# Performance work log

Hardware: AMD Instinct MI355X
Metric: run time of the kernel (lower is better)

Reference implementation:

```python
import jax, jax.numpy as jnp
import numpy as np

N, E, H = 5000, 40000, 8
DIMS = [(258, 512), (516, 256), (262, 128), (136, 20)]  # (in_feature, out_feature) per GATDeformer


def setup_inputs() -> dict:
    key = jax.random.key(0)
    ks = jax.random.split(key, 10)
    s = 0.05
    data = jax.random.normal(ks[0], (N, 10), jnp.float32)
    src = jax.random.randint(ks[1], (E,), 0, N)
    off = jax.random.randint(ks[2], (E,), 1, N)
    edge_idx = jnp.stack([src, (src + off) % N]).astype(jnp.int32)  # no self loops by construction
    inp = {
        'data': data,
        'edge_idx': edge_idx,
        'W0': jax.random.normal(ks[3], (10, 256), jnp.float32) * s,
        'b0': jnp.zeros((256,), jnp.float32),
    }
    for i, (din, dout) in enumerate(DIMS, start=1):
        k = jax.random.split(ks[3 + i], 3)
        inp[f'W{i}'] = jax.random.normal(k[0], (din, H * dout), jnp.float32) * s
        inp[f'asrc{i}'] = jax.random.normal(k[1], (H, dout), jnp.float32) * s
        inp[f'adst{i}'] = jax.random.normal(k[2], (H, dout), jnp.float32) * s
        inp[f'bias{i}'] = jnp.zeros((dout,), jnp.float32)
    return inp


def _gat(x, src, dst, W, a_s, a_d, b):
    """PyG GATConv (concat=False): returns (mean-over-heads output + bias, alpha [E',H])."""
    Hh, C = a_s.shape
    h = (x @ W).reshape(N, Hh, C)                               # [N,H,C]
    e_s = jnp.einsum('nhc,hc->nh', h, a_s)                      # [N,H]
    e_d = jnp.einsum('nhc,hc->nh', h, a_d)
    logits = jax.nn.leaky_relu(e_s[src] + e_d[dst], 0.2)        # [E',H]
    m = jax.ops.segment_max(logits, dst, num_segments=N)        # segment softmax over incoming edges
    ex = jnp.exp(logits - m[dst])
    alpha = ex / jax.ops.segment_sum(ex, dst, num_segments=N)[dst]
    out = jax.ops.segment_sum(alpha[:, :, None] * h[src], dst, num_segments=N)  # [N,H,C]
    return out.mean(axis=1) + b, alpha


def _deformer(af, src, dst, W, a_s, a_d, b):
    # find_boundary on the layer input features
    up, down = af[:, 0] == 1.0, af[:, 0] == 0.0
    left, right = af[:, 1] == 0.0, af[:, 1] == 1.0
    feat, alpha = _gat(af, src, dst, W, a_s, a_d, b)
    coord = af[:, :2]
    # second propagate: alpha*0.2 reused to aggregate source coordinates, then mean over heads
    msg = (alpha * 0.2)[:, :, None] * coord[src][:, None, :]    # [E',H,2]
    oc = jax.ops.segment_sum(msg, dst, num_segments=N).mean(axis=1)
    # fix_boundary (sequential overwrite order: up then down, left then right)
    c0 = jnp.where(down, 0.0, jnp.where(up, 1.0, oc[:, 0]))
    c1 = jnp.where(right, 1.0, jnp.where(left, 0.0, oc[:, 1]))
    return jnp.stack([c0, c1], axis=1), jax.nn.selu(feat)


def reference(data, edge_idx, W0, b0, W1, asrc1, adst1, bias1, W2, asrc2, adst2, bias2, W3, asrc3, adst3, bias3, W4, asrc4, adst4, bias4):
    sl = jnp.arange(N, dtype=edge_idx.dtype)
    src = jnp.concatenate([edge_idx[0], sl])   # GATConv add_self_loops=True
    dst = jnp.concatenate([edge_idx[1], sl])
    coord = data[:, :2]
    feat = jax.nn.selu(data @ W0 + b0)
    c1_, f1 = _deformer(jnp.concatenate([coord, feat], 1), src, dst, W1, asrc1, adst1, bias1)
    c2_, f2 = _deformer(jnp.concatenate([c1_, coord, f1], 1), src, dst, W2, asrc2, adst2, bias2)
    c3_, f3 = _deformer(jnp.concatenate([c2_, c1_, coord, f2], 1), src, dst, W3, asrc3, adst3, bias3)
    c4_, _ = _deformer(jnp.concatenate([c3_, c2_, c1_, coord, f3], 1), src, dst, W4, asrc4, adst4, bias4)
    return c4_
```

## Files before the change

### kernel.cpp

```cpp
#include <hip/hip_runtime.h>

#define N_NODES 5000
#define NH 8
#define MAXDEG 128

typedef unsigned short u16;
typedef short bf16x8 __attribute__((ext_vector_type(8)));
typedef float f32x4 __attribute__((ext_vector_type(4)));

static __device__ __forceinline__ float selu_f(float x) {
    const float sc = 1.0507009873554805f;
    const float al = 1.6732632423543772f;
    return x > 0.f ? sc * x : sc * al * (__expf(x) - 1.f);
}

static __device__ __forceinline__ u16 f2bf(float x) {
    union { float f; unsigned u; } v; v.f = x;
    unsigned r = v.u + 0x7fff + ((v.u >> 16) & 1);
    return (u16)(r >> 16);
}

static __device__ __forceinline__ float bf2f(unsigned hi16) {
    union { unsigned u; float f; } v; v.u = hi16 << 16;
    return v.f;
}

#define GL2LDS16(gp, lp)                                                        \
    __builtin_amdgcn_global_load_lds(                                           \
        (const __attribute__((address_space(1))) void*)(gp),                    \
        (__attribute__((address_space(3))) void*)(lp), 16, 0, 0)

#define WAVE_LDS_FENCE() asm volatile("s_waitcnt lgkmcnt(0)" ::: "memory")

__global__ __launch_bounds__(256) void k_prep(
        const float* W1, const float* W2, const float* W3, const float* W4,
        const float* s1, const float* s2, const float* s3, const float* s4,
        const float* d1, const float* d2, const float* d3, const float* d4,
        float* __restrict__ fsAll, float* __restrict__ fdAll,
        u16* T1, u16* T2, u16* T3, int* __restrict__ cnt) {
    const int Ks[4] = {258, 516, 262, 136};
    const int Cs[4] = {512, 256, 128, 20};
    const int NB0 = 16 * 18;
    const int NB1 = 8  * 34;
    const int NB2 = 4  * 18;
    const int NWTR = NB0 + NB1 + NB2;
    int bid = blockIdx.x;
    if (bid < 516) {
        int li = bid / 129;
        int k = (bid % 129) * 4 + (threadIdx.x >> 6);
        int lane = threadIdx.x & 63;
        if (k >= Ks[li]) return;
        const float* W  = (li == 0) ? W1 : (li == 1) ? W2 : (li == 2) ? W3 : W4;
        const float* as = (li == 0) ? s1 : (li == 1) ? s2 : (li == 2) ? s3 : s4;
        const float* ad = (li == 0) ? d1 : (li == 1) ? d2 : (li == 2) ? d3 : d4;
        int C = Cs[li];
        float s[8] = {0.f,0.f,0.f,0.f,0.f,0.f,0.f,0.f};
        float d[8] = {0.f,0.f,0.f,0.f,0.f,0.f,0.f,0.f};
        const float* wr = W + (size_t)k * 8 * C;
        for (int c = lane * 4; c < C; c += 256) {
            #pragma unroll
            for (int h = 0; h < 8; ++h) {
                float4 wv = *(const float4*)(wr + h * C + c);
                float4 sv = *(const float4*)(as + h * C + c);
                float4 dv = *(const float4*)(ad + h * C + c);
                s[h] += wv.x * sv.x + wv.y * sv.y + wv.z * sv.z + wv.w * sv.w;
                d[h] += wv.x * dv.x + wv.y * dv.y + wv.z * dv.z + wv.w * dv.w;
            }
        }
        #pragma unroll
        for (int off = 32; off >= 1; off >>= 1) {
            #pragma unroll
            for (int h = 0; h < 8; ++h) {
                s[h] += __shfl_xor(s[h], off);
                d[h] += __shfl_xor(d[h], off);
            }
        }
        if (lane == 0) {
            float* fo = fsAll + (size_t)li * 516 * 8 + k * 8;
            float* go = fdAll + (size_t)li * 516 * 8 + k * 8;
            #pragma unroll
            for (int h = 0; h < 8; ++h) { fo[h] = s[h]; go[h] = d[h]; }
        }
    } else if (bid < 516 + NWTR) {
        int w = bid - 516;
        int li, rem, nc;
        if (w < NB0)            { li = 0; rem = w;             nc = 16; }
        else if (w < NB0 + NB1) { li = 1; rem = w - NB0;       nc = 8;  }
        else                    { li = 2; rem = w - NB0 - NB1; nc = 4;  }
        const int Kps[3] = {288, 544, 288};
        int C = Cs[li], K = Ks[li], Kp = Kps[li], KK = 8 * Kp;
        int c0 = (rem % nc) * 32;
        int jb = (rem / nc) * 128;
        const float* W = (li == 0) ? W1 : (li == 1) ? W2 : W3;
        u16* Wt2 = (li == 0) ? T1 : (li == 1) ? T2 : T3;
        __shared__ float tile[32][33];
        int t = threadIdx.x;
        int kr = t >> 3, f = t & 7;
        #pragma unroll
        for (int jt = 0; jt < 4; ++jt) {
            int j0 = jb + jt * 32;
            int h = j0 / Kp, k0 = j0 % Kp;
            int gk = k0 + kr;
            float4 v = {0.f, 0.f, 0.f, 0.f};
            if (gk < K) v = *(const float4*)(W + (size_t)gk * (8 * C) + h * C + c0 + f * 4);
            tile[kr][f * 4 + 0] = v.x;
            tile[kr][f * 4 + 1] = v.y;
            tile[kr][f * 4 + 2] = v.z;
            tile[kr][f * 4 + 3] = v.w;
            __syncthreads();
            int cr = kr, kc0 = f * 4;
            ushort4 o;
            o.x = f2bf(tile[kc0 + 0][cr]);
            o.y = f2bf(tile[kc0 + 1][cr]);
            o.z = f2bf(tile[kc0 + 2][cr]);
            o.w = f2bf(tile[kc0 + 3][cr]);
            *(ushort4*)(Wt2 + (size_t)(c0 + cr) * KK + j0 + kc0) = o;
            __syncthreads();
        }
    } else {
        for (int i = threadIdx.x; i < N_NODES; i += 256) cnt[i] = 0;
    }
}

__global__ __launch_bounds__(256) void k_fmf1b(
        const int* __restrict__ ei, int* __restrict__ cnt,
        int* __restrict__ ssrcb, int E, int Esz, int gE,
        const float* __restrict__ data, const float* __restrict__ W0,
        const float* __restrict__ b0,
        const float* __restrict__ fs, const float* __restrict__ fd,
        u16* __restrict__ afb, float* __restrict__ es, float* __restrict__ ed,
        float* __restrict__ c0out) {
    int bid = blockIdx.x, t = threadIdx.x;
    if (bid < gE) {
        int e = bid * 256 + t;
        if (e >= Esz) return;
        int src, dst;
        if (e < E) { src = ei[e]; dst = ei[E + e]; }
        else       { src = e - E; dst = src; }
        int pos = atomicAdd(&cnt[dst], 1);
        if (pos < MAXDEG) ssrcb[dst * MAXDEG + pos] = src;
        return;
    }
    const int FC = 256, K = 258, Kp = 288;
    int n = bid - gE;
    __shared__ float drow[10];
    if (t < 10) drow[t] = data[n * 10 + t];
    __syncthreads();
    float pes[8] = {0.f,0.f,0.f,0.f,0.f,0.f,0.f,0.f};
    float ped[8] = {0.f,0.f,0.f,0.f,0.f,0.f,0.f,0.f};
    u16* rowb = afb + (size_t)n * Kp;
    for (int cf2 = t; 2 * cf2 < FC; cf2 += 256) {
        int cf = 2 * cf2;
        float2 bb = *(const float2*)(b0 + cf);
        float v0 = bb.x, v1 = bb.y;
        #pragma unroll
        for (int k = 0; k < 10; ++k) {
            float2 ww = *(const float2*)(W0 + k * 256 + cf);
            v0 += drow[k] * ww.x;
            v1 += drow[k] * ww.y;
        }
        v0 = selu_f(v0); v1 = selu_f(v1);
        int c = 2 + cf;
        *(unsigned*)(rowb + c) = (unsigned)f2bf(v0) | ((unsigned)f2bf(v1) << 16);
        const float* fsr = fs + c * 8;
        const float* fdr = fd + c * 8;
        #pragma unroll
        for (int h = 0; h < 8; ++h) {
            pes[h] += v0 * fsr[h] + v1 * fsr[8 + h];
            ped[h] += v0 * fdr[h] + v1 * fdr[8 + h];
        }
    }
    if (t < 2) {
        float v = drow[t];
        c0out[n * 2 + t] = v;
        rowb[t] = f2bf(v);
        #pragma unroll
        for (int h = 0; h < 8; ++h) { pes[h] += v * fs[t * 8 + h]; ped[h] += v * fd[t * 8 + h]; }
    }
    for (int c = K + t; c < Kp; c += 256) rowb[c] = 0;
    #pragma unroll
    for (int off = 32; off >= 1; off >>= 1) {
        #pragma unroll
        for (int h = 0; h < 8; ++h) {
            pes[h] += __shfl_xor(pes[h], off);
            ped[h] += __shfl_xor(ped[h], off);
        }
    }
    __shared__ float red[4][16];
    int wv = t >> 6, ln = t & 63;
    if (ln == 0) {
        #pragma unroll
        for (int h = 0; h < 8; ++h) { red[wv][h] = pes[h]; red[wv][8 + h] = ped[h]; }
    }
    __syncthreads();
    if (t < 16) {
        float s = red[0][t] + red[1][t] + red[2][t] + red[3][t];
        if (t < 8) es[n * 8 + t] = s;
        else       ed[n * 8 + (t - 8)] = s;
    }
}

__global__ __launch_bounds__(256) void k_mf(const float* p0, const float* p1,
                                            const float* p2, const float* p3, int np,
                                            const u16* __restrict__ facc,
                                            const float* __restrict__ biasp,
                                            int split, int MN, int FC, int K, int Kp,
                                            const float* __restrict__ fs,
                                            const float* __restrict__ fd,
                                            u16* __restrict__ afb,
                                            float* __restrict__ es, float* __restrict__ ed) {
    int n = blockIdx.x, t = threadIdx.x;
    float pes[8] = {0.f,0.f,0.f,0.f,0.f,0.f,0.f,0.f};
    float ped[8] = {0.f,0.f,0.f,0.f,0.f,0.f,0.f,0.f};
    u16* rowb = afb + (size_t)n * Kp;
    for (int cf2 = t; 2 * cf2 < FC; cf2 += 256) {
        int cf = 2 * cf2;
        float s0 = 0.f, s1 = 0.f;
        for (int z = 0; z < split; ++z) {
            unsigned pr = *(const unsigned*)(facc + (size_t)z * MN + (size_t)n * FC + cf);
            s0 += bf2f(pr & 0xffff);
            s1 += bf2f(pr >> 16);
        }
        float2 bb = *(const float2*)(biasp + cf);
        float v0 = selu_f(s0 * 0.125f + bb.x);
        float v1 = selu_f(s1 * 0.125f + bb.y);
        int c = 2 * np + cf;
        *(unsigned*)(rowb + c) = (unsigned)f2bf(v0) | ((unsigned)f2bf(v1) << 16);
        const float* fsr = fs + c * 8;
        const float* fdr = fd + c * 8;
        #pragma unroll
        for (int h = 0; h < 8; ++h) {
            pes[h] += v0 * fsr[h] + v1 * fsr[8 + h];
            ped[h] += v0 * fdr[h] + v1 * fdr[8 + h];
        }
    }
    if (t < 2 * np) {
        const float* p = (t < 2) ? p0 : (t < 4) ? p1 : (t < 6) ? p2 : p3;
        float v = p[n * 2 + (t & 1)];
        rowb[t] = f2bf(v);
        #pragma unroll
        for (int h = 0; h < 8; ++h) { pes[h] += v * fs[t * 8 + h]; ped[h] += v * fd[t * 8 + h]; }
    }
    for (int c = K + t; c < Kp; c += 256) rowb[c] = 0;
    #pragma unroll
    for (int off = 32; off >= 1; off >>= 1) {
        #pragma unroll
        for (int h = 0; h < 8; ++h) {
            pes[h] += __shfl_xor(pes[h], off);
            ped[h] += __shfl_xor(ped[h], off);
        }
    }
    __shared__ float red[4][16];
    int wv = t >> 6, ln = t & 63;
    if (ln == 0) {
        #pragma unroll
        for (int h = 0; h < 8; ++h) { red[wv][h] = pes[h]; red[wv][8 + h] = ped[h]; }
    }
    __syncthreads();
    if (t < 16) {
        float s = red[0][t] + red[1][t] + red[2][t] + red[3][t];
        if (t < 8) es[n * 8 + t] = s;
        else       ed[n * 8 + (t - 8)] = s;
    }
}

template <int S>
__global__ __launch_bounds__(256) void k_gag2(const float* __restrict__ es,
                            const float* __restrict__ ed,
                            const int* __restrict__ cnt, const int* __restrict__ ssrcb,
                            const float* __restrict__ cprev, const u16* __restrict__ afb,
                            u16* __restrict__ g, float* __restrict__ cnext, int Kp) {
    __shared__ float la_s[4][128 * 8];
    __shared__ int   ls_s[4][128];
    __shared__ float linv_s[4][8];
    int w4 = threadIdx.x >> 6, lane = threadIdx.x & 63;
    int n = blockIdx.x * 4 + w4;
    if (n >= N_NODES) return;
    float* la = la_s[w4];
    int*   ls = ls_s[w4];
    float* linv = linv_s[w4];

    int deg = cnt[n];
    if (deg > MAXDEG) deg = MAXDEG;
    const int* row = ssrcb + (size_t)n * MAXDEG;
    for (int i = lane; i < deg; i += 64) ls[i] = row[i];
    WAVE_LDS_FENCE();

    int h = lane & 7, ei = lane >> 3;
    float edh = ed[n * 8 + h];
    float m = -1e30f;
    for (int b = 0; b < deg; b += 8) {
        int e = b + ei;
        if (e < deg) {
            float x = es[ls[e] * 8 + h] + edh;
            x = x > 0.f ? x : 0.2f * x;
            la[e * 8 + h] = x;
            m = fmaxf(m, x);
        }
    }
    m = fmaxf(m, __shfl_xor(m, 8));
    m = fmaxf(m, __shfl_xor(m, 16));
    m = fmaxf(m, __shfl_xor(m, 32));
    WAVE_LDS_FENCE();
    float ssum = 0.f;
    for (int b = 0; b < deg; b += 8) {
        int e = b + ei;
        if (e < deg) {
            float v = __expf(la[e * 8 + h] - m);
            la[e * 8 + h] = v;
            ssum += v;
        }
    }
    ssum += __shfl_xor(ssum, 8);
    ssum += __shfl_xor(ssum, 16);
    ssum += __shfl_xor(ssum, 32);
    if (lane < 8) linv[lane] = 1.f / ssum;
    WAVE_LDS_FENCE();

    int nW = Kp >> 1;
    float linv8[8];
    #pragma unroll
    for (int h2 = 0; h2 < 8; ++h2) linv8[h2] = linv[h2];

    float acc[8][2 * S];
    #pragma unroll
    for (int h2 = 0; h2 < 8; ++h2)
        #pragma unroll
        for (int s = 0; s < 2 * S; ++s) acc[h2][s] = 0.f;
    int e = 0;
    for (; e + 3 < deg; e += 4) {
        const unsigned* r0 = (const unsigned*)(afb + (size_t)ls[e] * Kp);
        const unsigned* r1 = (const unsigned*)(afb + (size_t)ls[e + 1] * Kp);
        const unsigned* r2 = (const unsigned*)(afb + (size_t)ls[e + 2] * Kp);
        const unsigned* r3 = (const unsigned*)(afb + (size_t)ls[e + 3] * Kp);
        unsigned v0[S], v1[S], v2[S], v3[S];
        #pragma unroll
        for (int s = 0; s < S; ++s) {
            int w = lane + 64 * s;
            bool ok = (w < nW);
            v0[s] = ok ? r0[w] : 0u;
            v1[s] = ok ? r1[w] : 0u;
            v2[s] = ok ? r2[w] : 0u;
            v3[s] = ok ? r3[w] : 0u;
        }
        float a0[8], a1[8], a2[8], a3[8];
        #pragma unroll
        for (int h2 = 0; h2 < 8; ++h2) {
            a0[h2] = la[(e + 0) * 8 + h2];
            a1[h2] = la[(e + 1) * 8 + h2];
            a2[h2] = la[(e + 2) * 8 + h2];
            a3[h2] = la[(e + 3) * 8 + h2];
        }
        #pragma unroll
        for (int s = 0; s < S; ++s) {
            float x0 = bf2f(v0[s] & 0xffff), y0 = bf2f(v0[s] >> 16);
            float x1 = bf2f(v1[s] & 0xffff), y1 = bf2f(v1[s] >> 16);
            float x2 = bf2f(v2[s] & 0xffff), y2 = bf2f(v2[s] >> 16);
            float x3 = bf2f(v3[s] & 0xffff), y3 = bf2f(v3[s] >> 16);
            #pragma unroll
            for (int h2 = 0; h2 < 8; ++h2) {
                acc[h2][2 * s]     += a0[h2] * x0 + a1[h2] * x1 + a2[h2] * x2 + a3[h2] * x3;
                acc[h2][2 * s + 1] += a0[h2] * y0 + a1[h2] * y1 + a2[h2] * y2 + a3[h2] * y3;
            }
        }
    }
    for (; e < deg; ++e) {
        const unsigned* r0 = (const unsigned*)(afb + (size_t)ls[e] * Kp);
        unsigned v0[S];
        #pragma unroll
        for (int s = 0; s < S; ++s) {
            int w = lane + 64 * s;
            v0[s] = (w < nW) ? r0[w] : 0u;
        }
        float a0[8];
        #pragma unroll
        for (int h2 = 0; h2 < 8; ++h2) a0[h2] = la[e * 8 + h2];
        #pragma unroll
        for (int s = 0; s < S; ++s) {
            float x0 = bf2f(v0[s] & 0xffff), y0 = bf2f(v0[s] >> 16);
            #pragma unroll
            for (int h2 = 0; h2 < 8; ++h2) {
                acc[h2][2 * s]     += a0[h2] * x0;
                acc[h2][2 * s + 1] += a0[h2] * y0;
            }
        }
    }
    unsigned* grw = (unsigned*)(g + (size_t)n * 8 * Kp);
    #pragma unroll
    for (int s = 0; s < S; ++s) {
        int w = lane + 64 * s;
        if (w < nW) {
            #pragma unroll
            for (int h2 = 0; h2 < 8; ++h2) {
                float iv = linv8[h2];
                unsigned lo = f2bf(acc[h2][2 * s] * iv);
                unsigned hi = f2bf(acc[h2][2 * s + 1] * iv);
                grw[h2 * nW + w] = lo | (hi << 16);
            }
        }
    }
    float oc0 = 0.f, oc1 = 0.f;
    for (int i = lane; i < deg; i += 64) {
        float wsum = 0.f;
        #pragma unroll
        for (int h2 = 0; h2 < 8; ++h2) wsum += la[i * 8 + h2] * linv8[h2];
        int src = ls[i];
        oc0 += wsum * cprev[src * 2];
        oc1 += wsum * cprev[src * 2 + 1];
    }
    #pragma unroll
    for (int off = 1; off <= 32; off <<= 1) {
        oc0 += __shfl_xor(oc0, off);
        oc1 += __shfl_xor(oc1, off);
    }
    if (lane == 0) {
        oc0 *= 0.025f; oc1 *= 0.025f;
        float a0 = cprev[n * 2], a1 = cprev[n * 2 + 1];
        cnext[n * 2]     = (a0 == 0.f) ? 0.f : ((a0 == 1.f) ? 1.f : oc0);
        cnext[n * 2 + 1] = (a1 == 1.f) ? 1.f : ((a1 == 0.f) ? 0.f : oc1);
    }
}

__global__ __launch_bounds__(256) void k_gemm_s(const u16* __restrict__ A,
                                                const u16* __restrict__ Bt,
                                                u16* __restrict__ facc16,
                                                int M, int KK, int NC, int kchunk, int MN) {
    __shared__ u16 As[3][128 * 32];
    __shared__ u16 Bs[3][128 * 32];
    int tid = threadIdx.x;
    int wave = tid >> 6, lane = tid & 63;
    int bm = blockIdx.y * 128, bn = blockIdx.x * 128, z = blockIdx.z;
    int kbeg = z * kchunk, kend = min(KK, kbeg + kchunk);
    int wm = (wave >> 1) * 64, wn = (wave & 1) * 64;
    int l16 = lane & 15, q = lane >> 4;
    f32x4 acc[4][4] = {};

    int seg0 = wave * 128 + lane;
    int seg1 = seg0 + 64;
    int row0 = seg0 >> 2, sq0 = (seg0 & 3) ^ (row0 & 3);
    int row1 = seg1 >> 2, sq1 = (seg1 & 3) ^ (row1 & 3);
    const u16* ga0 = A  + (size_t)(bm + row0) * KK + sq0 * 8;
    const u16* ga1 = A  + (size_t)(bm + row1) * KK + sq1 * 8;
    const u16* gb0 = Bt + (size_t)(bn + row0) * KK + sq0 * 8;
    const u16* gb1 = Bt + (size_t)(bn + row1) * KK + sq1 * 8;
    int lo0 = (wave * 2 + 0) * 512;
    int lo1 = (wave * 2 + 1) * 512;

#define STAGE_T(buf, kk)                          \
    do {                                          \
        GL2LDS16(ga0 + (kk), &As[buf][lo0]);      \
        GL2LDS16(ga1 + (kk), &As[buf][lo1]);      \
        GL2LDS16(gb0 + (kk), &Bs[buf][lo0]);      \
        GL2LDS16(gb1 + (kk), &Bs[buf][lo1]);      \
    } while (0)

    STAGE_T(0, kbeg);
    if (kbeg + 32 < kend) STAGE_T(1, kbeg + 32);
    int cur = 0;
    for (int k0 = kbeg; k0 < kend; k0 += 32) {
        if (k0 + 64 < kend) {
            int nb = cur + 2; if (nb >= 3) nb -= 3;
            STAGE_T(nb, k0 + 64);
            asm volatile("s_waitcnt vmcnt(8)" ::: "memory");
        } else if (k0 + 32 < kend) {
            asm volatile("s_waitcnt vmcnt(4)" ::: "memory");
        } else {
            asm volatile("s_waitcnt vmcnt(0)" ::: "memory");
        }
        __builtin_amdgcn_s_barrier();
        const u16* Asr = As[cur];
        const u16* Bsr = Bs[cur];
        bf16x8 fa[4], fb[4];
        #pragma unroll
        for (int mi = 0; mi < 4; ++mi) {
            int row = wm + mi * 16 + l16;
            fa[mi] = *(const bf16x8*)(Asr + row * 32 + ((q ^ (row & 3)) * 8));
            int col = wn + mi * 16 + l16;
            fb[mi] = *(const bf16x8*)(Bsr + col * 32 + ((q ^ (col & 3)) * 8));
        }
        #pragma unroll
        for (int mi = 0; mi < 4; ++mi)
            #pragma unroll
            for (int ni = 0; ni < 4; ++ni)
                acc[mi][ni] = __builtin_amdgcn_mfma_f32_16x16x32_bf16(fa[mi], fb[ni], acc[mi][ni], 0, 0, 0);
        __builtin_amdgcn_s_barrier();
        cur += 1; if (cur >= 3) cur -= 3;
    }
#undef STAGE_T
    u16* out = facc16 + (size_t)z * MN;
    #pragma unroll
    for (int mi = 0; mi < 4; ++mi) {
        int row0s = bm + wm + mi * 16 + q * 4;
        #pragma unroll
        for (int ni = 0; ni < 4; ++ni) {
            int col = bn + wn + ni * 16 + l16;
            #pragma unroll
            for (int r = 0; r < 4; ++r) {
                int row = row0s + r;
                if (row < M) out[(size_t)row * NC + col] = f2bf(acc[mi][ni][r]);
            }
        }
    }
}

__global__ void k_final(const float* __restrict__ es, const float* __restrict__ ed,
                        const int* __restrict__ cnt, const int* __restrict__ ssrcb,
                        const float* __restrict__ cprev, float* __restrict__ outp) {
    int wid = (blockIdx.x * blockDim.x + threadIdx.x) >> 6;
    int lane = threadIdx.x & 63;
    if (wid >= N_NODES) return;
    int n = wid;
    int deg = cnt[n];
    if (deg > MAXDEG) deg = MAXDEG;
    const int* row = ssrcb + (size_t)n * MAXDEG;
    int h = lane & 7, ei = lane >> 3;
    float edh = ed[n * 8 + h];
    float m = -1e30f;
    for (int b = 0; b < deg; b += 8) {
        int e = b + ei;
        if (e < deg) {
            int src = row[e];
            float x = es[src * 8 + h] + edh;
            x = x > 0.f ? x : 0.2f * x;
            m = fmaxf(m, x);
        }
    }
    m = fmaxf(m, __shfl_xor(m, 8));
    m = fmaxf(m, __shfl_xor(m, 16));
    m = fmaxf(m, __shfl_xor(m, 32));
    float ssum = 0.f;
    for (int b = 0; b < deg; b += 8) {
        int e = b + ei;
        if (e < deg) {
            int src = row[e];
            float x = es[src * 8 + h] + edh;
            x = x > 0.f ? x : 0.2f * x;
            ssum += __expf(x - m);
        }
    }
    ssum += __shfl_xor(ssum, 8);
    ssum += __shfl_xor(ssum, 16);
    ssum += __shfl_xor(ssum, 32);
    float inv = 1.f / ssum;
    float oc0 = 0.f, oc1 = 0.f;
    for (int b = 0; b < deg; b += 8) {
        int e = b + ei;
        if (e < deg) {
            int src = row[e];
            float x = es[src * 8 + h] + edh;
            x = x > 0.f ? x : 0.2f * x;
            float w = __expf(x - m) * inv;
            w += __shfl_xor(w, 1);
            w += __shfl_xor(w, 2);
            w += __shfl_xor(w, 4);
            if (h == 0) {
                oc0 += w * cprev[src * 2];
                oc1 += w * cprev[src * 2 + 1];
            }
        }
    }
    oc0 += __shfl_xor(oc0, 8);  oc1 += __shfl_xor(oc1, 8);
    oc0 += __shfl_xor(oc0, 16); oc1 += __shfl_xor(oc1, 16);
    oc0 += __shfl_xor(oc0, 32); oc1 += __shfl_xor(oc1, 32);
    if (lane == 0) {
        oc0 *= 0.025f; oc1 *= 0.025f;
        float a0 = cprev[n * 2], a1 = cprev[n * 2 + 1];
        outp[n * 2]     = (a0 == 0.f) ? 0.f : ((a0 == 1.f) ? 1.f : oc0);
        outp[n * 2 + 1] = (a1 == 1.f) ? 1.f : ((a1 == 0.f) ? 0.f : oc1);
    }
}

extern "C" void kernel_launch(void* const* d_in, const int* in_sizes, int n_in,
                              void* d_out, int out_size, void* d_ws, size_t ws_size,
                              hipStream_t stream) {
    const float* data = (const float*)d_in[0];
    const int* ei = (const int*)d_in[1];
    const float* W0 = (const float*)d_in[2];
    const float* b0 = (const float*)d_in[3];
    int E = in_sizes[1] / 2;
    int Esz = E + N_NODES;
    int gE = (Esz + 255) / 256;

    char* wp = (char*)d_ws;
    size_t off = 0;
    auto alloc = [&](size_t bytes) {
        void* p = wp + off;
        off += (bytes + 1023) & ~(size_t)1023;
        return p;
    };
    u16*   g     = (u16*)alloc((size_t)N_NODES * 8 * 576 * 2);
    u16*   T1    = (u16*)alloc((size_t)512 * 8 * 288 * 2);
    u16*   T2    = (u16*)alloc((size_t)256 * 8 * 544 * 2);
    u16*   T3    = (u16*)alloc((size_t)128 * 8 * 288 * 2);
    u16*   facc  = (u16*)alloc((size_t)8 * N_NODES * 512 * 2);
    u16*   afb   = (u16*)alloc((size_t)N_NODES * 576 * 2);
    float* es    = (float*)alloc((size_t)N_NODES * 8 * 4);
    float* ebd   = (float*)alloc((size_t)N_NODES * 8 * 4);
    float* fsAll = (float*)alloc((size_t)4 * 516 * 8 * 4);
    float* fdAll = (float*)alloc((size_t)4 * 516 * 8 * 4);
    float* c0    = (float*)alloc(N_NODES * 2 * 4);
    float* c1    = (float*)alloc(N_NODES * 2 * 4);
    float* c2    = (float*)alloc(N_NODES * 2 * 4);
    float* c3    = (float*)alloc(N_NODES * 2 * 4);
    int* cnt   = (int*)alloc(N_NODES * 4);
    int* ssrcb = (int*)alloc((size_t)N_NODES * MAXDEG * 4);

    struct LP { const float *W, *as, *ad, *bs; int K, C, split; };
    LP L[4] = {
        {(const float*)d_in[4],  (const float*)d_in[5],  (const float*)d_in[6],  (const float*)d_in[7],  258, 512, 4},
        {(const float*)d_in[8],  (const float*)d_in[9],  (const float*)d_in[10], (const float*)d_in[11], 516, 256, 8},
        {(const float*)d_in[12], (const float*)d_in[13], (const float*)d_in[14], (const float*)d_in[15], 262, 128, 8},
        {(const float*)d_in[16], (const float*)d_in[17], (const float*)d_in[18], (const float*)d_in[19], 136, 20, 1},
    };

    k_prep<<<516 + 632 + 1, 256, 0, stream>>>(
        L[0].W, L[1].W, L[2].W, L[3].W,
        L[0].as, L[1].as, L[2].as, L[3].as,
        L[0].ad, L[1].ad, L[2].ad, L[3].ad,
        fsAll, fdAll, T1, T2, T3, cnt);

    k_fmf1b<<<gE + N_NODES, 256, 0, stream>>>(
        ei, cnt, ssrcb, E, Esz, gE,
        data, W0, b0,
        fsAll + 0, fdAll + 0, afb, es, ebd, c0);

    float* cbuf[4] = {c0, c1, c2, c3};
    u16* Tb[3] = {T1, T2, T3};
    int FC[4] = {256, 512, 256, 128};

    for (int li = 0; li < 4; ++li) {
        LP& lp = L[li];
        int Kp = ((lp.K + 31) / 32) * 32;
        int KK = 8 * Kp;

        if (li >= 1) {
            const float* p[4] = {nullptr, nullptr, nullptr, nullptr};
            for (int j = 0; j <= li; ++j) p[j] = cbuf[li - j];
            const float* biasp = L[li - 1].bs;
            int splitp = L[li - 1].split;
            int MNp = N_NODES * FC[li];
            const float* fs = fsAll + (size_t)li * 516 * 8;
            const float* fd = fdAll + (size_t)li * 516 * 8;
            k_mf<<<N_NODES, 256, 0, stream>>>(p[0], p[1], p[2], p[3], li + 1,
                                              facc, biasp, splitp, MNp, FC[li],
                                              lp.K, Kp, fs, fd, afb, es, ebd);
        }
        if (li < 3) {
            int gG = (N_NODES + 3) / 4;
            if (Kp == 544)
                k_gag2<5><<<gG, 256, 0, stream>>>(es, ebd, cnt, ssrcb, cbuf[li], afb,
                                                  g, cbuf[li + 1], Kp);
            else
                k_gag2<3><<<gG, 256, 0, stream>>>(es, ebd, cnt, ssrcb, cbuf[li], afb,
                                                  g, cbuf[li + 1], Kp);
            int MN = N_NODES * lp.C;
            k_gemm_s<<<dim3(lp.C / 128, (N_NODES + 127) / 128, lp.split), 256, 0, stream>>>(
                g, Tb[li], facc, N_NODES, KK, lp.C, KK / lp.split, MN);
        } else {
            k_final<<<(N_NODES + 3) / 4, 256, 0, stream>>>(es, ebd, cnt, ssrcb, cbuf[3],
                                                           (float*)d_out);
        }
    }
}
```

Baseline: 330.6 us.

## Fuse bias/SELU/attention-logit epilogue into GEMM and drop split-K buffer

Removes the separate k_mf kernel and the split-K bf16 partial buffer. The GEMM now runs without K splitting, with a tile-order remap. Its epilogue applies bias and SELU, writes the next layer's bf16 features, and accumulates per-head source/destination logits via shuffles and atomicAdd. The aggregation kernel now computes the coordinate part of the next layer's logits and input row, with ping-pong buffers for features and logits. This saves a launch and a large round-trip through global memory. In exchange, grids without split-K have fewer blocks (as few as 40 for the last layer), the epilogue uses atomics, and the atomic targets rely on being initialized by the aggregation kernel, which adds an ordering dependency.

```diff
diff --git a/kernel.cpp b/kernel.cpp
--- a/kernel.cpp
+++ b/kernel.cpp
@@ -200,76 +200,17 @@
     }
 }
 
-__global__ __launch_bounds__(256) void k_mf(const float* p0, const float* p1,
-                                            const float* p2, const float* p3, int np,
-                                            const u16* __restrict__ facc,
-                                            const float* __restrict__ biasp,
-                                            int split, int MN, int FC, int K, int Kp,
-                                            const float* __restrict__ fs,
-                                            const float* __restrict__ fd,
-                                            u16* __restrict__ afb,
-                                            float* __restrict__ es, float* __restrict__ ed) {
-    int n = blockIdx.x, t = threadIdx.x;
-    float pes[8] = {0.f,0.f,0.f,0.f,0.f,0.f,0.f,0.f};
-    float ped[8] = {0.f,0.f,0.f,0.f,0.f,0.f,0.f,0.f};
-    u16* rowb = afb + (size_t)n * Kp;
-    for (int cf2 = t; 2 * cf2 < FC; cf2 += 256) {
-        int cf = 2 * cf2;
-        float s0 = 0.f, s1 = 0.f;
-        for (int z = 0; z < split; ++z) {
-            unsigned pr = *(const unsigned*)(facc + (size_t)z * MN + (size_t)n * FC + cf);
-            s0 += bf2f(pr & 0xffff);
-            s1 += bf2f(pr >> 16);
-        }
-        float2 bb = *(const float2*)(biasp + cf);
-        float v0 = selu_f(s0 * 0.125f + bb.x);
-        float v1 = selu_f(s1 * 0.125f + bb.y);
-        int c = 2 * np + cf;
-        *(unsigned*)(rowb + c) = (unsigned)f2bf(v0) | ((unsigned)f2bf(v1) << 16);
-        const float* fsr = fs + c * 8;
-        const float* fdr = fd + c * 8;
-        #pragma unroll
-        for (int h = 0; h < 8; ++h) {
-            pes[h] += v0 * fsr[h] + v1 * fsr[8 + h];
-            ped[h] += v0 * fdr[h] + v1 * fdr[8 + h];
-        }
-    }
-    if (t < 2 * np) {
-        const float* p = (t < 2) ? p0 : (t < 4) ? p1 : (t < 6) ? p2 : p3;
-        float v = p[n * 2 + (t & 1)];
-        rowb[t] = f2bf(v);
-        #pragma unroll
-        for (int h = 0; h < 8; ++h) { pes[h] += v * fs[t * 8 + h]; ped[h] += v * fd[t * 8 + h]; }
-    }
-    for (int c = K + t; c < Kp; c += 256) rowb[c] = 0;
-    #pragma unroll
-    for (int off = 32; off >= 1; off >>= 1) {
-        #pragma unroll
-        for (int h = 0; h < 8; ++h) {
-            pes[h] += __shfl_xor(pes[h], off);
-            ped[h] += __shfl_xor(ped[h], off);
-        }
-    }
-    __shared__ float red[4][16];
-    int wv = t >> 6, ln = t & 63;
-    if (ln == 0) {
-        #pragma unroll
-        for (int h = 0; h < 8; ++h) { red[wv][h] = pes[h]; red[wv][8 + h] = ped[h]; }
-    }
-    __syncthreads();
-    if (t < 16) {
-        float s = red[0][t] + red[1][t] + red[2][t] + red[3][t];
-        if (t < 8) es[n * 8 + t] = s;
-        else       ed[n * 8 + (t - 8)] = s;
-    }
-}
-
 template <int S>
-__global__ __launch_bounds__(256) void k_gag2(const float* __restrict__ es,
+__global__ __launch_bounds__(256) void k_gag3(const float* __restrict__ es,
                             const float* __restrict__ ed,
                             const int* __restrict__ cnt, const int* __restrict__ ssrcb,
                             const float* __restrict__ cprev, const u16* __restrict__ afb,
-                            u16* __restrict__ g, float* __restrict__ cnext, int Kp) {
+                            u16* __restrict__ g, float* __restrict__ cnext, int Kp,
+                            int np1, int K1, int Kp1,
+                            const float* __restrict__ fs1, const float* __restrict__ fd1,
+                            float* __restrict__ esN, float* __restrict__ edN,
+                            u16* __restrict__ afbN,
+                            const float* __restrict__ p2, const float* __restrict__ p3) {
     __shared__ float la_s[4][128 * 8];
     __shared__ int   ls_s[4][128];
     __shared__ float linv_s[4][8];
@@ -413,24 +354,54 @@
         oc0 += __shfl_xor(oc0, off);
         oc1 += __shfl_xor(oc1, off);
     }
-    if (lane == 0) {
-        oc0 *= 0.025f; oc1 *= 0.025f;
-        float a0 = cprev[n * 2], a1 = cprev[n * 2 + 1];
-        cnext[n * 2]     = (a0 == 0.f) ? 0.f : ((a0 == 1.f) ? 1.f : oc0);
-        cnext[n * 2 + 1] = (a1 == 1.f) ? 1.f : ((a1 == 0.f) ? 0.f : oc1);
-    }
-}
-
-__global__ __launch_bounds__(256) void k_gemm_s(const u16* __restrict__ A,
+    float a0 = cprev[n * 2], a1 = cprev[n * 2 + 1];
+    float cn0 = (a0 == 0.f) ? 0.f : ((a0 == 1.f) ? 1.f : oc0 * 0.025f);
+    float cn1 = (a1 == 1.f) ? 1.f : ((a1 == 0.f) ? 0.f : oc1 * 0.025f);
+    if (lane == 0) { cnext[n * 2] = cn0; cnext[n * 2 + 1] = cn1; }
+    float cv[8];
+    cv[0] = cn0; cv[1] = cn1;
+    cv[2] = a0;  cv[3] = a1;
+    cv[4] = 0.f; cv[5] = 0.f; cv[6] = 0.f; cv[7] = 0.f;
+    if (np1 >= 3) { cv[4] = p2[n * 2]; cv[5] = p2[n * 2 + 1]; }
+    if (np1 >= 4) { cv[6] = p3[n * 2]; cv[7] = p3[n * 2 + 1]; }
+    if (lane < 8) {
+        float se = 0.f, sd = 0.f;
+        for (int t2 = 0; t2 < 2 * np1; ++t2) {
+            se += cv[t2] * fs1[t2 * 8 + lane];
+            sd += cv[t2] * fd1[t2 * 8 + lane];
+        }
+        esN[n * 8 + lane] = se;
+        edN[n * 8 + lane] = sd;
+    }
+    if (afbN) {
+        if (lane < 2 * np1) afbN[(size_t)n * Kp1 + lane] = f2bf(cv[lane]);
+        for (int c = K1 + lane; c < Kp1; c += 64) afbN[(size_t)n * Kp1 + c] = 0;
+    }
+}
+
+__global__ __launch_bounds__(256) void k_gemm_f(const u16* __restrict__ A,
                                                 const u16* __restrict__ Bt,
-                                                u16* __restrict__ facc16,
-                                                int M, int KK, int NC, int kchunk, int MN) {
+                                                int M, int KK, int NC, int nbx,
+                                                const float* __restrict__ bias,
+                                                int np1, int Kp1,
+                                                const float* __restrict__ fs1,
+                                                const float* __restrict__ fd1,
+                                                float* __restrict__ esN,
+                                                float* __restrict__ edN,
+                                                u16* __restrict__ afbN) {
     __shared__ u16 As[3][128 * 32];
     __shared__ u16 Bs[3][128 * 32];
     int tid = threadIdx.x;
     int wave = tid >> 6, lane = tid & 63;
-    int bm = blockIdx.y * 128, bn = blockIdx.x * 128, z = blockIdx.z;
-    int kbeg = z * kchunk, kend = min(KK, kbeg + kchunk);
+
+    int T = gridDim.x;
+    int per8 = T >> 3;
+    int o = blockIdx.x;
+    int oo = (o & 7) * per8 + (o >> 3);
+    int by = oo / nbx;
+    int bx = oo - by * nbx;
+
+    int bm = by * 128, bn = bx * 128;
     int wm = (wave >> 1) * 64, wn = (wave & 1) * 64;
     int l16 = lane & 15, q = lane >> 4;
     f32x4 acc[4][4] = {};
@@ -454,15 +425,15 @@
         GL2LDS16(gb1 + (kk), &Bs[buf][lo1]);      \
     } while (0)
 
-    STAGE_T(0, kbeg);
-    if (kbeg + 32 < kend) STAGE_T(1, kbeg + 32);
+    STAGE_T(0, 0);
+    if (32 < KK) STAGE_T(1, 32);
     int cur = 0;
-    for (int k0 = kbeg; k0 < kend; k0 += 32) {
-        if (k0 + 64 < kend) {
+    for (int k0 = 0; k0 < KK; k0 += 32) {
+        if (k0 + 64 < KK) {
             int nb = cur + 2; if (nb >= 3) nb -= 3;
             STAGE_T(nb, k0 + 64);
             asm volatile("s_waitcnt vmcnt(8)" ::: "memory");
-        } else if (k0 + 32 < kend) {
+        } else if (k0 + 32 < KK) {
             asm volatile("s_waitcnt vmcnt(4)" ::: "memory");
         } else {
             asm volatile("s_waitcnt vmcnt(0)" ::: "memory");
@@ -487,17 +458,46 @@
         cur += 1; if (cur >= 3) cur -= 3;
     }
 #undef STAGE_T
-    u16* out = facc16 + (size_t)z * MN;
+    int base = 2 * np1;
     #pragma unroll
     for (int mi = 0; mi < 4; ++mi) {
-        int row0s = bm + wm + mi * 16 + q * 4;
-        #pragma unroll
-        for (int ni = 0; ni < 4; ++ni) {
-            int col = bn + wn + ni * 16 + l16;
-            #pragma unroll
-            for (int r = 0; r < 4; ++r) {
-                int row = row0s + r;
-                if (row < M) out[(size_t)row * NC + col] = f2bf(acc[mi][ni][r]);
+        #pragma unroll
+        for (int r = 0; r < 4; ++r) {
+            int row = bm + wm + mi * 16 + q * 4 + r;
+            bool okrow = (row < M);
+            float pe[8] = {0.f,0.f,0.f,0.f,0.f,0.f,0.f,0.f};
+            float pd[8] = {0.f,0.f,0.f,0.f,0.f,0.f,0.f,0.f};
+            #pragma unroll
+            for (int ni = 0; ni < 4; ++ni) {
+                int cf = bn + wn + ni * 16 + l16;
+                float v = selu_f(acc[mi][ni][r] * 0.125f + bias[cf]);
+                if (okrow && afbN)
+                    afbN[(size_t)row * Kp1 + base + cf] = f2bf(v);
+                const float* fr = fs1 + (size_t)(base + cf) * 8;
+                const float* dr = fd1 + (size_t)(base + cf) * 8;
+                float4 fra = *(const float4*)(fr);
+                float4 frb = *(const float4*)(fr + 4);
+                float4 dra = *(const float4*)(dr);
+                float4 drb = *(const float4*)(dr + 4);
+                pe[0] += v * fra.x; pe[1] += v * fra.y; pe[2] += v * fra.z; pe[3] += v * fra.w;
+                pe[4] += v * frb.x; pe[5] += v * frb.y; pe[6] += v * frb.z; pe[7] += v * frb.w;
+                pd[0] += v * dra.x; pd[1] += v * dra.y; pd[2] += v * dra.z; pd[3] += v * dra.w;
+                pd[4] += v * drb.x; pd[5] += v * drb.y; pd[6] += v * drb.z; pd[7] += v * drb.w;
+            }
+            #pragma unroll
+            for (int off = 1; off <= 8; off <<= 1) {
+                #pragma unroll
+                for (int h = 0; h < 8; ++h) {
+                    pe[h] += __shfl_xor(pe[h], off);
+                    pd[h] += __shfl_xor(pd[h], off);
+                }
+            }
+            if (okrow && l16 == 0) {
+                #pragma unroll
+                for (int h = 0; h < 8; ++h) {
+                    atomicAdd(&esN[row * 8 + h], pe[h]);
+                    atomicAdd(&edN[row * 8 + h], pd[h]);
+                }
             }
         }
     }
@@ -592,10 +592,12 @@
     u16*   T1    = (u16*)alloc((size_t)512 * 8 * 288 * 2);
     u16*   T2    = (u16*)alloc((size_t)256 * 8 * 544 * 2);
     u16*   T3    = (u16*)alloc((size_t)128 * 8 * 288 * 2);
-    u16*   facc  = (u16*)alloc((size_t)8 * N_NODES * 512 * 2);
-    u16*   afb   = (u16*)alloc((size_t)N_NODES * 576 * 2);
-    float* es    = (float*)alloc((size_t)N_NODES * 8 * 4);
-    float* ebd   = (float*)alloc((size_t)N_NODES * 8 * 4);
+    u16*   afbA  = (u16*)alloc((size_t)N_NODES * 576 * 2);
+    u16*   afbB  = (u16*)alloc((size_t)N_NODES * 576 * 2);
+    float* esA   = (float*)alloc((size_t)N_NODES * 8 * 4);
+    float* esB   = (float*)alloc((size_t)N_NODES * 8 * 4);
+    float* edA   = (float*)alloc((size_t)N_NODES * 8 * 4);
+    float* edB   = (float*)alloc((size_t)N_NODES * 8 * 4);
     float* fsAll = (float*)alloc((size_t)4 * 516 * 8 * 4);
     float* fdAll = (float*)alloc((size_t)4 * 516 * 8 * 4);
     float* c0    = (float*)alloc(N_NODES * 2 * 4);
@@ -605,13 +607,20 @@
     int* cnt   = (int*)alloc(N_NODES * 4);
     int* ssrcb = (int*)alloc((size_t)N_NODES * MAXDEG * 4);
 
-    struct LP { const float *W, *as, *ad, *bs; int K, C, split; };
+    struct LP { const float *W, *as, *ad, *bs; int K, C; };
     LP L[4] = {
-        {(const float*)d_in[4],  (const float*)d_in[5],  (const float*)d_in[6],  (const float*)d_in[7],  258, 512, 4},
-        {(const float*)d_in[8],  (const float*)d_in[9],  (const float*)d_in[10], (const float*)d_in[11], 516, 256, 8},
-        {(const float*)d_in[12], (const float*)d_in[13], (const float*)d_in[14], (const float*)d_in[15], 262, 128, 8},
-        {(const float*)d_in[16], (const float*)d_in[17], (const float*)d_in[18], (const float*)d_in[19], 136, 20, 1},
+        {(const float*)d_in[4],  (const float*)d_in[5],  (const float*)d_in[6],  (const float*)d_in[7],  258, 512},
+        {(const float*)d_in[8],  (const float*)d_in[9],  (const float*)d_in[10], (const float*)d_in[11], 516, 256},
+        {(const float*)d_in[12], (const float*)d_in[13], (const float*)d_in[14], (const float*)d_in[15], 262, 128},
+        {(const float*)d_in[16], (const float*)d_in[17], (const float*)d_in[18], (const float*)d_in[19], 136, 20},
     };
+
+    u16*   afb2[2] = {afbA, afbB};
+    float* esb[2]  = {esA, esB};
+    float* edb[2]  = {edA, edB};
+    float* cbuf[4] = {c0, c1, c2, c3};
+    u16* Tb[3] = {T1, T2, T3};
+    const int KpL[4] = {288, 544, 288, 160};
 
     k_prep<<<516 + 632 + 1, 256, 0, stream>>>(
         L[0].W, L[1].W, L[2].W, L[3].W,
@@ -622,43 +631,44 @@
     k_fmf1b<<<gE + N_NODES, 256, 0, stream>>>(
         ei, cnt, ssrcb, E, Esz, gE,
         data, W0, b0,
-        fsAll + 0, fdAll + 0, afb, es, ebd, c0);
-
-    float* cbuf[4] = {c0, c1, c2, c3};
-    u16* Tb[3] = {T1, T2, T3};
-    int FC[4] = {256, 512, 256, 128};
-
-    for (int li = 0; li < 4; ++li) {
-        LP& lp = L[li];
-        int Kp = ((lp.K + 31) / 32) * 32;
-        int KK = 8 * Kp;
-
-        if (li >= 1) {
-            const float* p[4] = {nullptr, nullptr, nullptr, nullptr};
-            for (int j = 0; j <= li; ++j) p[j] = cbuf[li - j];
-            const float* biasp = L[li - 1].bs;
-            int splitp = L[li - 1].split;
-            int MNp = N_NODES * FC[li];
-            const float* fs = fsAll + (size_t)li * 516 * 8;
-            const float* fd = fdAll + (size_t)li * 516 * 8;
-            k_mf<<<N_NODES, 256, 0, stream>>>(p[0], p[1], p[2], p[3], li + 1,
-                                              facc, biasp, splitp, MNp, FC[li],
-                                              lp.K, Kp, fs, fd, afb, es, ebd);
-        }
-        if (li < 3) {
-            int gG = (N_NODES + 3) / 4;
-            if (Kp == 544)
-                k_gag2<5><<<gG, 256, 0, stream>>>(es, ebd, cnt, ssrcb, cbuf[li], afb,
-                                                  g, cbuf[li + 1], Kp);
-            else
-                k_gag2<3><<<gG, 256, 0, stream>>>(es, ebd, cnt, ssrcb, cbuf[li], afb,
-                                                  g, cbuf[li + 1], Kp);
-            int MN = N_NODES * lp.C;
-            k_gemm_s<<<dim3(lp.C / 128, (N_NODES + 127) / 128, lp.split), 256, 0, stream>>>(
-                g, Tb[li], facc, N_NODES, KK, lp.C, KK / lp.split, MN);
-        } else {
-            k_final<<<(N_NODES + 3) / 4, 256, 0, stream>>>(es, ebd, cnt, ssrcb, cbuf[3],
-                                                           (float*)d_out);
-        }
-    }
-}
+        fsAll + 0, fdAll + 0, afb2[1], esb[1], edb[1], c0);
+
+    for (int li = 0; li < 3; ++li) {
+        int l = li + 1;
+        int cu = l & 1, nx = (l + 1) & 1;
+        int KpC = KpL[li];
+        int KK = 8 * KpC;
+        int np1 = li + 2;
+        int K1  = (li < 2) ? L[li + 1].K : 0;
+        int Kp1 = (li < 2) ? KpL[li + 1] : 0;
+        const float* fs1 = fsAll + (size_t)(li + 1) * 516 * 8;
+        const float* fd1 = fdAll + (size_t)(li + 1) * 516 * 8;
+        u16* afbN = (li < 2) ? afb2[nx] : (u16*)nullptr;
+        const float* p2 = (np1 >= 3) ? cbuf[li - 1] : nullptr;
+        const float* p3 = (np1 >= 4) ? cbuf[li - 2] : nullptr;
+
+        int gG = (N_NODES + 3) / 4;
+        if (KpC == 544)
+            k_gag3<5><<<gG, 256, 0, stream>>>(esb[cu], edb[cu], cnt, ssrcb,
+                                              cbuf[li], afb2[cu], g, cbuf[li + 1], KpC,
+                                              np1, K1, Kp1, fs1, fd1,
+                                              esb[nx], edb[nx], afbN, p2, p3);
+        else
+            k_gag3<3><<<gG, 256, 0, stream>>>(esb[cu], edb[cu], cnt, ssrcb,
+                                              cbuf[li], afb2[cu], g, cbuf[li + 1], KpC,
+                                              np1, K1, Kp1, fs1, fd1,
+                                              esb[nx], edb[nx], afbN, p2, p3);
+
+        int NC = L[li].C;
+        int nbx = NC / 128;
+        int nby = (N_NODES + 127) / 128;
+        int ntile = nbx * nby;
+        k_gemm_f<<<ntile, 256, 0, stream>>>(
+            g, Tb[li], N_NODES, KK, NC, nbx,
+            L[li].bs, np1, Kp1, fs1, fd1,
+            esb[nx], edb[nx], afbN);
+    }
+
+    k_final<<<(N_NODES + 3) / 4, 256, 0, stream>>>(esb[0], edb[0], cnt, ssrcb, cbuf[3],
+                                                   (float*)d_out);
+}
```

Result: slower. 528.4 us (+59.8%).
